# Optimization experiments

Hardware: AMD Instinct MI355X
Metric: run time of the kernel (lower is better)

## Reference

```python
import jax, jax.numpy as jnp
import numpy as np


def _slopes(y, x):
    # Finite-difference slopes along the last axis, extended to length N:
    # one-sided at endpoints, averaged in the interior (standard Hermite tangents).
    m = (y[..., 1:] - y[..., :-1]) / (x[1:] - x[:-1])  # [..., N-1]
    return jnp.concatenate(
        [m[..., :1], 0.5 * (m[..., 1:] + m[..., :-1]), m[..., -1:]], axis=-1
    )  # [..., N]


def _interp1d(y, x0, m, xs):
    # y, m: [..., N]; x0: [N] sorted; xs: [Q] queries -> [..., Q]
    I = jnp.searchsorted(x0[1:-1], xs)          # bucket index in [0, N-2]
    x_lo = x0[I]
    dx = x0[I + 1] - x_lo
    t = (xs - x_lo) / dx
    t2 = t * t
    t3 = t2 * t
    h00 = 1.0 - 3.0 * t2 + 2.0 * t3   # A row 0: [1,0,-3,2]
    h10 = t - 2.0 * t2 + t3           # A row 1: [0,1,-2,1]
    h01 = 3.0 * t2 - 2.0 * t3         # A row 2: [0,0,3,-2]
    h11 = t3 - t2                     # A row 3: [0,0,-1,1]
    y_lo = jnp.take(y, I, axis=-1)
    y_hi = jnp.take(y, I + 1, axis=-1)
    m_lo = jnp.take(m, I, axis=-1)
    m_hi = jnp.take(m, I + 1, axis=-1)
    return h00 * y_lo + h10 * m_lo * dx + h01 * y_hi + h11 * m_hi * dx


def setup_inputs() -> dict:
    key = jax.random.key(0)
    k_sig, k_xs, k_ys = jax.random.split(key, 3)
    B, H, W = 32, 512, 512
    Nx, Ny = 1024, 1024
    signal = jax.random.normal(k_sig, (B, H, W), dtype=jnp.float32)
    x1 = jnp.arange(W, dtype=jnp.float32)  # sorted axis for last dim
    x2 = jnp.arange(H, dtype=jnp.float32)  # sorted axis for second-to-last dim
    xs = jnp.sort(jax.random.uniform(k_xs, (Nx,), dtype=jnp.float32) * (W - 1))
    ys = jnp.sort(jax.random.uniform(k_ys, (Ny,), dtype=jnp.float32) * (H - 1))
    return {"signal": signal, "x1": x1, "x2": x2, "xs": xs, "ys": ys}


def reference(signal, x1, x2, xs, ys):
    # Pass 1: interpolate along W at xs -> [B, H, Nx]
    m1 = _slopes(signal, x1)
    out = _interp1d(signal, x1, m1, xs)
    # Pass 2: interpolate along H at ys (operate on transposed data) -> [B, Nx, Ny]
    out_t = jnp.swapaxes(out, -1, -2)   # [B, Nx, H]
    m2 = _slopes(out_t, x2)
    out2 = _interp1d(out_t, x2, m2, ys)
    return jnp.swapaxes(out2, -1, -2)   # [B, Ny, Nx]
```

## Files before the change

### kernel.cpp

```cpp
#include <hip/hip_runtime.h>

#define B_  32
#define H_  512
#define W_  512
#define NX_ 1024
#define NY_ 1024
#define R_  8
#define STG 11
#define SW  516

__device__ __forceinline__ void hermite_window(float x, int N, int& c0, float4& v) {
    int i = (int)floorf(x);
    i = min(max(i, 0), N - 2);
    float t  = x - (float)i;
    float t2 = t * t;
    float t3 = t2 * t;
    float h00 = 1.0f - 3.0f * t2 + 2.0f * t3;
    float h10 = t - 2.0f * t2 + t3;
    float h01 = 3.0f * t2 - 2.0f * t3;
    float h11 = t3 - t2;
    if (i == 0) {
        c0 = 0;
        v = make_float4(h00 - h10 - 0.5f * h11,
                        h01 + h10,
                        0.5f * h11,
                        0.0f);
    } else if (i == N - 2) {
        c0 = i - 1;
        v = make_float4(-0.5f * h10,
                        h00 - h11,
                        h01 + 0.5f * h10 + h11,
                        0.0f);
    } else {
        c0 = i - 1;
        v = make_float4(-0.5f * h10,
                        h00 - 0.5f * h11,
                        h01 + 0.5f * h10,
                        0.5f * h11);
    }
}

__global__ void prep_tables(const float* __restrict__ xs, const float* __restrict__ ys,
                            float4* __restrict__ wxw, int* __restrict__ cx0,
                            float4* __restrict__ wyw, int* __restrict__ ry0) {
    int q = blockIdx.x * blockDim.x + threadIdx.x;
    if (q < NX_) {
        int c; float4 w;
        hermite_window(xs[q], W_, c, w);
        wxw[q] = w; cx0[q] = c;
    } else if (q < NX_ + NY_) {
        int qq = q - NX_;
        int c; float4 w;
        hermite_window(ys[qq], H_, c, w);
        wyw[qq] = w; ry0[qq] = c;
    }
}

__global__ __launch_bounds__(256) void fused(
    const float* __restrict__ sig,
    const float* __restrict__ ys,
    const float4* __restrict__ wxw, const int* __restrict__ cx0,
    const float4* __restrict__ wyw, const int* __restrict__ ry0,
    float* __restrict__ out)
{
    __shared__ float stage[STG][SW];
    const int tid = threadIdx.x;
    const int qx0 = blockIdx.x * 256;
    const int r0  = blockIdx.y * R_;
    const int b   = blockIdx.z;

    const float* sb = sig + (size_t)b * H_ * W_;
    for (int j = tid; j < STG * (SW / 4); j += 256) {
        int s  = j / (SW / 4);
        int c4 = j - s * (SW / 4);
        int gr = min(max(r0 - 1 + s, 0), H_ - 1);
        float4 val = (c4 < W_ / 4) ? ((const float4*)(sb + (size_t)gr * W_))[c4]
                                   : make_float4(0.f, 0.f, 0.f, 0.f);
        *(float4*)&stage[s][c4 * 4] = val;
    }
    __syncthreads();

    const int qx = qx0 + tid;
    const float4 w = wxw[qx];
    const int c0 = cx0[qx];
    float c[STG];
    #pragma unroll
    for (int s = 0; s < STG; ++s) {
        const float* sr = stage[s];
        c[s] = w.x * sr[c0] + w.y * sr[c0 + 1] + w.z * sr[c0 + 2] + w.w * sr[c0 + 3];
    }

    int lo = 0, hi = NY_;
    const float fl = (float)r0;
    while (lo < hi) { int m = (lo + hi) >> 1; lo = (ys[m] < fl) ? m + 1 : lo, hi = (ys[m] < fl) ? hi : m; }
    const int qyA = lo;
    hi = NY_;
    const float fh = (float)(r0 + R_);
    while (lo < hi) { int m = (lo + hi) >> 1; lo = (ys[m] < fh) ? m + 1 : lo, hi = (ys[m] < fh) ? hi : m; }
    const int qyB = lo;

    float* ob = out + (size_t)b * NY_ * NX_ + qx;
    for (int qy = qyA; qy < qyB; ++qy) {
        float4 wv = wyw[qy];
        int s0 = ry0[qy] - r0 + 1;
        s0 = __builtin_amdgcn_readfirstlane(s0);
        float acc;
        switch (s0) {
            case 0: acc = wv.x*c[0] + wv.y*c[1] + wv.z*c[2]  + wv.w*c[3];  break;
            case 1: acc = wv.x*c[1] + wv.y*c[2] + wv.z*c[3]  + wv.w*c[4];  break;
            case 2: acc = wv.x*c[2] + wv.y*c[3] + wv.z*c[4]  + wv.w*c[5];  break;
            case 3: acc = wv.x*c[3] + wv.y*c[4] + wv.z*c[5]  + wv.w*c[6];  break;
            case 4: acc = wv.x*c[4] + wv.y*c[5] + wv.z*c[6]  + wv.w*c[7];  break;
            case 5: acc = wv.x*c[5] + wv.y*c[6] + wv.z*c[7]  + wv.w*c[8];  break;
            case 6: acc = wv.x*c[6] + wv.y*c[7] + wv.z*c[8]  + wv.w*c[9];  break;
            case 7: acc = wv.x*c[7] + wv.y*c[8] + wv.z*c[9]  + wv.w*c[10]; break;
            default: acc = 0.0f; break;
        }
        ob[(size_t)qy * NX_] = acc;
    }
}

extern "C" void kernel_launch(void* const* d_in, const int* in_sizes, int n_in,
                              void* d_out, int out_size, void* d_ws, size_t ws_size,
                              hipStream_t stream) {
    const float* signal = (const float*)d_in[0];
    const float* xs = (const float*)d_in[3];
    const float* ys = (const float*)d_in[4];
    float* out = (float*)d_out;

    float4* wxw = (float4*)d_ws;
    float4* wyw = wxw + NX_;
    int* cx0 = (int*)(wyw + NY_);
    int* ry0 = cx0 + NX_;

    prep_tables<<<(NX_ + NY_ + 255) / 256, 256, 0, stream>>>(xs, ys, wxw, cx0, wyw, ry0);

    dim3 grid(NX_ / 256, H_ / R_, B_);
    fused<<<grid, 256, 0, stream>>>(signal, ys, wxw, cx0, wyw, ry0, out);
}
```

Before: 207.1 us.

## Give each thread four x-queries so blocks cover full rows and store float4

Each block now covers all 1024 x-queries for one row band, with every thread computing four adjacent x outputs. This removes the 4x redundant staging of the same signal rows into shared memory across x-blocks, and the output store becomes a 16-byte float4 write. The per-block binary searches over ys move into the prep kernel as precomputed band bounds. The y weights for each band are cached in shared memory. The cost is four times the register state per thread (11 float4 accumulators) and a quarter as many blocks (2048), which may lower occupancy and latency hiding.

```diff
diff --git a/kernel.cpp b/kernel.cpp
--- a/kernel.cpp
+++ b/kernel.cpp
@@ -6,8 +6,18 @@
 #define NX_ 1024
 #define NY_ 1024
 #define R_  8
-#define STG 11
+#define NB  (H_ / R_)
+#define STG (R_ + 3)
 #define SW  516
+#define MAXQ 64
+
+__device__ __forceinline__ float4 f4mul(float s, float4 a) {
+    return make_float4(s * a.x, s * a.y, s * a.z, s * a.w);
+}
+__device__ __forceinline__ float4 f4fma(float s, float4 a, float4 acc) {
+    acc.x += s * a.x; acc.y += s * a.y; acc.z += s * a.z; acc.w += s * a.w;
+    return acc;
+}
 
 __device__ __forceinline__ void hermite_window(float x, int N, int& c0, float4& v) {
     int i = (int)floorf(x);
@@ -21,28 +31,20 @@
     float h11 = t3 - t2;
     if (i == 0) {
         c0 = 0;
-        v = make_float4(h00 - h10 - 0.5f * h11,
-                        h01 + h10,
-                        0.5f * h11,
-                        0.0f);
+        v = make_float4(h00 - h10 - 0.5f * h11, h01 + h10, 0.5f * h11, 0.0f);
     } else if (i == N - 2) {
         c0 = i - 1;
-        v = make_float4(-0.5f * h10,
-                        h00 - h11,
-                        h01 + 0.5f * h10 + h11,
-                        0.0f);
+        v = make_float4(-0.5f * h10, h00 - h11, h01 + 0.5f * h10 + h11, 0.0f);
     } else {
         c0 = i - 1;
-        v = make_float4(-0.5f * h10,
-                        h00 - 0.5f * h11,
-                        h01 + 0.5f * h10,
-                        0.5f * h11);
+        v = make_float4(-0.5f * h10, h00 - 0.5f * h11, h01 + 0.5f * h10, 0.5f * h11);
     }
 }
 
 __global__ void prep_tables(const float* __restrict__ xs, const float* __restrict__ ys,
                             float4* __restrict__ wxw, int* __restrict__ cx0,
-                            float4* __restrict__ wyw, int* __restrict__ ry0) {
+                            float4* __restrict__ wyw, int* __restrict__ ry0,
+                            int* __restrict__ bandA, int* __restrict__ bandB) {
     int q = blockIdx.x * blockDim.x + threadIdx.x;
     if (q < NX_) {
         int c; float4 w;
@@ -53,21 +55,38 @@
         int c; float4 w;
         hermite_window(ys[qq], H_, c, w);
         wyw[qq] = w; ry0[qq] = c;
+    } else if (q < NX_ + NY_ + 2 * NB) {
+        int k = q - NX_ - NY_;
+        int isB = (k >= NB) ? 1 : 0;
+        int band = k - isB * NB;
+        float bound = (float)((band + isB) * R_);
+        int lo = 0, hi = NY_;
+        while (lo < hi) {
+            int m = (lo + hi) >> 1;
+            if (ys[m] < bound) lo = m + 1; else hi = m;
+        }
+        if (isB) bandB[band] = lo; else bandA[band] = lo;
     }
 }
 
 __global__ __launch_bounds__(256) void fused(
     const float* __restrict__ sig,
-    const float* __restrict__ ys,
     const float4* __restrict__ wxw, const int* __restrict__ cx0,
     const float4* __restrict__ wyw, const int* __restrict__ ry0,
+    const int* __restrict__ bandA, const int* __restrict__ bandB,
     float* __restrict__ out)
 {
     __shared__ float stage[STG][SW];
-    const int tid = threadIdx.x;
-    const int qx0 = blockIdx.x * 256;
-    const int r0  = blockIdx.y * R_;
-    const int b   = blockIdx.z;
+    __shared__ float4 wy_s[MAXQ];
+    __shared__ int   slot_s[MAXQ];
+
+    const int tid  = threadIdx.x;
+    const int band = blockIdx.x;
+    const int b    = blockIdx.y;
+    const int r0   = band * R_;
+
+    const int qyA = bandA[band];
+    const int nq  = bandB[band] - qyA;
 
     const float* sb = sig + (size_t)b * H_ * W_;
     for (int j = tid; j < STG * (SW / 4); j += 256) {
@@ -78,45 +97,43 @@
                                    : make_float4(0.f, 0.f, 0.f, 0.f);
         *(float4*)&stage[s][c4 * 4] = val;
     }
+    if (tid < nq && tid < MAXQ) {
+        int qy = qyA + tid;
+        wy_s[tid]   = wyw[qy];
+        slot_s[tid] = ry0[qy] - r0 + 1;
+    }
     __syncthreads();
 
-    const int qx = qx0 + tid;
-    const float4 w = wxw[qx];
-    const int c0 = cx0[qx];
-    float c[STG];
+    const int qxb = tid * 4;
+    const float4 w0 = wxw[qxb], w1 = wxw[qxb + 1], w2 = wxw[qxb + 2], w3 = wxw[qxb + 3];
+    const int4 ci = *(const int4*)(cx0 + qxb);
+    float4 c[STG];
     #pragma unroll
     for (int s = 0; s < STG; ++s) {
         const float* sr = stage[s];
-        c[s] = w.x * sr[c0] + w.y * sr[c0 + 1] + w.z * sr[c0 + 2] + w.w * sr[c0 + 3];
+        c[s].x = w0.x * sr[ci.x] + w0.y * sr[ci.x + 1] + w0.z * sr[ci.x + 2] + w0.w * sr[ci.x + 3];
+        c[s].y = w1.x * sr[ci.y] + w1.y * sr[ci.y + 1] + w1.z * sr[ci.y + 2] + w1.w * sr[ci.y + 3];
+        c[s].z = w2.x * sr[ci.z] + w2.y * sr[ci.z + 1] + w2.z * sr[ci.z + 2] + w2.w * sr[ci.z + 3];
+        c[s].w = w3.x * sr[ci.w] + w3.y * sr[ci.w + 1] + w3.z * sr[ci.w + 2] + w3.w * sr[ci.w + 3];
     }
 
-    int lo = 0, hi = NY_;
-    const float fl = (float)r0;
-    while (lo < hi) { int m = (lo + hi) >> 1; lo = (ys[m] < fl) ? m + 1 : lo, hi = (ys[m] < fl) ? hi : m; }
-    const int qyA = lo;
-    hi = NY_;
-    const float fh = (float)(r0 + R_);
-    while (lo < hi) { int m = (lo + hi) >> 1; lo = (ys[m] < fh) ? m + 1 : lo, hi = (ys[m] < fh) ? hi : m; }
-    const int qyB = lo;
-
-    float* ob = out + (size_t)b * NY_ * NX_ + qx;
-    for (int qy = qyA; qy < qyB; ++qy) {
-        float4 wv = wyw[qy];
-        int s0 = ry0[qy] - r0 + 1;
+    float* ob = out + (size_t)b * NY_ * NX_ + qxb;
+    for (int j = 0; j < nq; ++j) {
+        float4 wv; int s0;
+        if (j < MAXQ) { wv = wy_s[j]; s0 = slot_s[j]; }
+        else { int qy = qyA + j; wv = wyw[qy]; s0 = ry0[qy] - r0 + 1; }
         s0 = __builtin_amdgcn_readfirstlane(s0);
-        float acc;
+        float4 acc;
+        #define CASE_(S) case S: \
+            acc = f4fma(wv.w, c[S + 3], f4fma(wv.z, c[S + 2], \
+                  f4fma(wv.y, c[S + 1], f4mul(wv.x, c[S])))); break;
         switch (s0) {
-            case 0: acc = wv.x*c[0] + wv.y*c[1] + wv.z*c[2]  + wv.w*c[3];  break;
-            case 1: acc = wv.x*c[1] + wv.y*c[2] + wv.z*c[3]  + wv.w*c[4];  break;
-            case 2: acc = wv.x*c[2] + wv.y*c[3] + wv.z*c[4]  + wv.w*c[5];  break;
-            case 3: acc = wv.x*c[3] + wv.y*c[4] + wv.z*c[5]  + wv.w*c[6];  break;
-            case 4: acc = wv.x*c[4] + wv.y*c[5] + wv.z*c[6]  + wv.w*c[7];  break;
-            case 5: acc = wv.x*c[5] + wv.y*c[6] + wv.z*c[7]  + wv.w*c[8];  break;
-            case 6: acc = wv.x*c[6] + wv.y*c[7] + wv.z*c[8]  + wv.w*c[9];  break;
-            case 7: acc = wv.x*c[7] + wv.y*c[8] + wv.z*c[9]  + wv.w*c[10]; break;
-            default: acc = 0.0f; break;
+            CASE_(0) CASE_(1) CASE_(2) CASE_(3)
+            CASE_(4) CASE_(5) CASE_(6) CASE_(7)
+            default: acc = make_float4(0.f, 0.f, 0.f, 0.f); break;
         }
-        ob[(size_t)qy * NX_] = acc;
+        #undef CASE_
+        *(float4*)(ob + (size_t)(qyA + j) * NX_) = acc;
     }
 }
 
@@ -130,11 +147,14 @@
 
     float4* wxw = (float4*)d_ws;
     float4* wyw = wxw + NX_;
-    int* cx0 = (int*)(wyw + NY_);
-    int* ry0 = cx0 + NX_;
+    int* cx0   = (int*)(wyw + NY_);
+    int* ry0   = cx0 + NX_;
+    int* bandA = ry0 + NY_;
+    int* bandB = bandA + NB;
 
-    prep_tables<<<(NX_ + NY_ + 255) / 256, 256, 0, stream>>>(xs, ys, wxw, cx0, wyw, ry0);
+    prep_tables<<<(NX_ + NY_ + 2 * NB + 255) / 256, 256, 0, stream>>>(
+        xs, ys, wxw, cx0, wyw, ry0, bandA, bandB);
 
-    dim3 grid(NX_ / 256, H_ / R_, B_);
-    fused<<<grid, 256, 0, stream>>>(signal, ys, wxw, cx0, wyw, ry0, out);
+    dim3 grid(NB, B_);
+    fused<<<grid, 256, 0, stream>>>(signal, wxw, cx0, wyw, ry0, bandA, bandB, out);
 }
```

Result: faster. 181.7 us (-12.2%).
